# Kernel optimization log

Hardware: AMD Instinct MI355X
Metric: run time of the kernel (lower is better)

The kernel has to match this reference:

```python
import jax, jax.numpy as jnp
import numpy as np

B, T = 32768, 32
OBJ_V, PRED_V = 179, 46
E_OBJ, E_PRED, H = 5, 5, 32
IN_DIM = E_OBJ + E_PRED + 2 + 4  # 16, matches LSTMCell input size


def setup_inputs() -> dict:
    key = jax.random.key(0)
    ks = jax.random.split(key, 12)
    s = 0.1
    return {
        "input_objects": jax.random.randint(ks[0], (B, T), 0, OBJ_V),
        "input_boxes": jax.random.uniform(ks[1], (B, T, 4), dtype=jnp.float32),
        "predicates": jax.random.randint(ks[2], (B, T), 0, PRED_V),
        "subject_indicators": jax.random.randint(ks[3], (B, T), 0, 2),
        "target_object": jax.random.randint(ks[4], (B,), 0, OBJ_V),
        "obj_emb": jax.random.normal(ks[5], (OBJ_V, E_OBJ), dtype=jnp.float32) * s,
        "pred_emb": jax.random.normal(ks[6], (PRED_V, E_PRED), dtype=jnp.float32) * s,
        "W_ih": jax.random.normal(ks[7], (4 * H, IN_DIM), dtype=jnp.float32) * s,
        "W_hh": jax.random.normal(ks[8], (4 * H, H), dtype=jnp.float32) * s,
        "b_ih": jnp.zeros((4 * H,), dtype=jnp.float32),
        "b_hh": jnp.zeros((4 * H,), dtype=jnp.float32),
        "fc2_W": jax.random.normal(ks[9], (4, H), dtype=jnp.float32) * s,
        "fc2_b": jnp.zeros((4,), dtype=jnp.float32),
    }


def _forward(input_objects, input_boxes, predicates, subject_indicators,
             obj_emb, pred_emb, W_ih, W_hh, b_ih, b_hh, fc2_W, fc2_b):
    # concatenate_features, vectorized over all timesteps at once: [B,T,16]
    feats = jnp.concatenate([
        obj_emb[input_objects],                                   # [B,T,5]
        pred_emb[predicates],                                     # [B,T,5]
        jax.nn.one_hot(subject_indicators, 2, dtype=jnp.float32), # [B,T,2]
        input_boxes,                                              # [B,T,4]
    ], axis=-1)
    xs = jnp.transpose(feats, (1, 0, 2))  # [T,B,16] for scan over time

    def step(carry, x):
        h, c = carry
        gates = x @ W_ih.T + b_ih + h @ W_hh.T + b_hh  # [B,4H]
        i, f, g, o = jnp.split(gates, 4, axis=-1)      # torch gate order i,f,g,o
        i = jax.nn.sigmoid(i)
        f = jax.nn.sigmoid(f)
        g = jnp.tanh(g)
        o = jax.nn.sigmoid(o)
        c = f * c + i * g
        h = o * jnp.tanh(c)
        return (h, c), None

    h0 = jnp.zeros((input_objects.shape[0], H), dtype=jnp.float32)
    (h, _), _ = jax.lax.scan(step, (h0, h0), xs)
    out = h @ fc2_W.T + fc2_b          # output_fc2 on last hidden state
    return jnp.clip(out, 0.0, 1.0)     # torch.clamp(min=0, max=1)


def reference(input_objects, input_boxes, predicates, subject_indicators, target_object,
              obj_emb, pred_emb, W_ih, W_hh, b_ih, b_hh, fc2_W, fc2_b):
    # target_object is accepted by the torch forward but unused in its body
    return _forward(input_objects, input_boxes, predicates, subject_indicators,
                    obj_emb, pred_emb, W_ih, W_hh, b_ih, b_hh, fc2_W, fc2_b)
```

## Files before the change

kernel.cpp:

```cpp
#include <hip/hip_runtime.h>

#define LDS_BYTES 16656

typedef _Float16 f16x8 __attribute__((ext_vector_type(8)));
typedef float    f32x4 __attribute__((ext_vector_type(4)));

#define LOG2E     1.44269504088896f
#define TWO_LOG2E 2.88539008177793f

__device__ __forceinline__ float sig_pre(float a) {
    return __builtin_amdgcn_rcpf(1.0f + __builtin_amdgcn_exp2f(a));
}
__device__ __forceinline__ float tanh_pre(float a) {
    return 1.0f - 2.0f * __builtin_amdgcn_rcpf(1.0f + __builtin_amdgcn_exp2f(a));
}
__device__ __forceinline__ int pack2(float a, float b) {
    union { _Float16 h[2]; int i; } u;
    u.h[0] = (_Float16)a; u.h[1] = (_Float16)b;
    return u.i;
}

__global__ __launch_bounds__(64, 2)
void lstm_fused(const int* __restrict__ objs,
                const float* __restrict__ boxes,
                const int* __restrict__ preds,
                const int* __restrict__ subj,
                const float* __restrict__ obj_emb,
                const float* __restrict__ pred_emb,
                const float* __restrict__ W_ih,
                const float* __restrict__ W_hh,
                const float* __restrict__ b_ih,
                const float* __restrict__ b_hh,
                const float* __restrict__ fc2_W,
                const float* __restrict__ fc2_b,
                float* __restrict__ out)
{
    extern __shared__ char smem[];
    const int tid  = threadIdx.x;
    const int quad = tid >> 4;
    const int cidx = tid & 15;
    const int XOFF = 0, ZOFF = 16640;

    if (tid < 4) ((int*)(smem + ZOFF))[tid] = 0;

    {
        int b  = tid >> 2;
        int t0 = (tid & 3) << 3;
        long gb = (long)blockIdx.x * 16 + b;
        const int* op = objs  + gb * 32 + t0;
        const int* pp = preds + gb * 32 + t0;
        const int* sp = subj  + gb * 32 + t0;
        #pragma unroll
        for (int c = 0; c < 8; c += 4) {
            int4 ov = *(const int4*)(op + c);
            int4 pv = *(const int4*)(pp + c);
            int4 sv = *(const int4*)(sp + c);
            int oarr[4] = {ov.x, ov.y, ov.z, ov.w};
            int parr[4] = {pv.x, pv.y, pv.z, pv.w};
            int sarr[4] = {sv.x, sv.y, sv.z, sv.w};
            #pragma unroll
            for (int tt = 0; tt < 4; ++tt) {
                int t = t0 + c + tt;
                const float* eo = obj_emb  + oarr[tt] * 5;
                const float* ep = pred_emb + parr[tt] * 5;
                float4 bx = *(const float4*)(boxes + (gb * 32 + t) * 4);
                f16x8 lo, hi;
                lo[0]=(_Float16)eo[0]; lo[1]=(_Float16)eo[1]; lo[2]=(_Float16)eo[2];
                lo[3]=(_Float16)eo[3]; lo[4]=(_Float16)eo[4];
                lo[5]=(_Float16)ep[0]; lo[6]=(_Float16)ep[1]; lo[7]=(_Float16)ep[2];
                hi[0]=(_Float16)ep[3]; hi[1]=(_Float16)ep[4];
                hi[2]=(_Float16)(sarr[tt]==0 ? 1.0f : 0.0f);
                hi[3]=(_Float16)(sarr[tt]==1 ? 1.0f : 0.0f);
                hi[4]=(_Float16)bx.x; hi[5]=(_Float16)bx.y;
                hi[6]=(_Float16)bx.z; hi[7]=(_Float16)bx.w;
                char* dst = smem + XOFF + b * 1040 + t * 32;
                *(f16x8*)dst        = lo;
                *(f16x8*)(dst + 16) = hi;
            }
        }
    }

    f16x8 Wf[8][2];
    f32x4 bias4[8];
    #pragma unroll
    for (int j = 0; j < 8; ++j) {
        float scale = (j == 4 || j == 5) ? TWO_LOG2E : -LOG2E;
        int n = j * 16 + cidx;
        #pragma unroll
        for (int ks = 0; ks < 2; ++ks) {
            f16x8 v;
            #pragma unroll
            for (int jj = 0; jj < 8; ++jj) {
                int k = ks * 32 + quad * 8 + jj;
                float val = (k < 16) ? W_ih[n * 16 + k]
                          : (k >= 32) ? W_hh[n * 32 + (k - 32)]
                          : 0.0f;
                v[jj] = (_Float16)(val * scale);
            }
            Wf[j][ks] = v;
        }
        #pragma unroll
        for (int r = 0; r < 4; ++r) {
            int nr = j * 16 + quad * 4 + r;
            bias4[j][r] = (b_ih[nr] + b_hh[nr]) * scale;
        }
    }

    const bool qlow = (quad < 2);
    int       xaddr = qlow ? (XOFF + cidx * 1040 + quad * 16) : ZOFF;
    const int xinc  = qlow ? 32 : 0;
    const int idx_lo = (((quad & 1) << 5) + cidx) << 2;
    const int idx_hi = idx_lo + 64;

    __syncthreads();

    f16x8 xfrag = *(const f16x8*)(smem + xaddr); xaddr += xinc;
    f32x4 accp[8];
    #pragma unroll
    for (int j = 0; j < 8; ++j)
        accp[j] = __builtin_amdgcn_mfma_f32_16x16x32_f16(Wf[j][0], xfrag, bias4[j], 0, 0, 0);

    int pkA = 0, pkB = 0, pkC = 0, pkD = 0;
    float cst[8] = {0,0,0,0,0,0,0,0};
    float hl[8];

    #pragma unroll 4
    for (int t = 0; t < 32; ++t) {
        int pa_lo = __builtin_amdgcn_ds_bpermute(idx_lo, pkA);
        int pb_lo = __builtin_amdgcn_ds_bpermute(idx_lo, pkB);
        int pa_hi = __builtin_amdgcn_ds_bpermute(idx_hi, pkA);
        int pb_hi = __builtin_amdgcn_ds_bpermute(idx_hi, pkB);
        int pc_lo = __builtin_amdgcn_ds_bpermute(idx_lo, pkC);
        int pd_lo = __builtin_amdgcn_ds_bpermute(idx_lo, pkD);
        int pc_hi = __builtin_amdgcn_ds_bpermute(idx_hi, pkC);
        int pd_hi = __builtin_amdgcn_ds_bpermute(idx_hi, pkD);
        union { int i[4]; f16x8 v; } hf;
        hf.i[0] = qlow ? pa_lo : pc_lo;
        hf.i[1] = qlow ? pb_lo : pd_lo;
        hf.i[2] = qlow ? pa_hi : pc_hi;
        hf.i[3] = qlow ? pb_hi : pd_hi;

        f32x4 acc[8];
        #pragma unroll
        for (int j = 0; j < 8; ++j)
            acc[j] = __builtin_amdgcn_mfma_f32_16x16x32_f16(Wf[j][1], hf.v, accp[j], 0, 0, 0);

        f16x8 xn = *(const f16x8*)(smem + xaddr); xaddr += xinc;

        #pragma unroll
        for (int r = 0; r < 4; ++r) {
            float si0 = sig_pre(acc[0][r]);
            float si1 = sig_pre(acc[1][r]);
            float sf0 = sig_pre(acc[2][r]);
            float sf1 = sig_pre(acc[3][r]);
            float tg0 = tanh_pre(acc[4][r]);
            float tg1 = tanh_pre(acc[5][r]);
            float so0 = sig_pre(acc[6][r]);
            float so1 = sig_pre(acc[7][r]);
            float c0 = fmaf(sf0, cst[2*r],   si0 * tg0);
            float c1 = fmaf(sf1, cst[2*r+1], si1 * tg1);
            cst[2*r] = c0; cst[2*r+1] = c1;
            hl[2*r]   = so0 * tanh_pre(c0 * TWO_LOG2E);
            hl[2*r+1] = so1 * tanh_pre(c1 * TWO_LOG2E);
        }
        pkA = pack2(hl[0], hl[2]);
        pkB = pack2(hl[4], hl[6]);
        pkC = pack2(hl[1], hl[3]);
        pkD = pack2(hl[5], hl[7]);

        #pragma unroll
        for (int j = 0; j < 8; ++j)
            accp[j] = __builtin_amdgcn_mfma_f32_16x16x32_f16(Wf[j][0], xn, bias4[j], 0, 0, 0);
    }

    __syncthreads();
    #pragma unroll
    for (int r = 0; r < 4; ++r) {
        *(float*)(smem + cidx * 144 + (quad * 4 + r) * 4)        = hl[2*r];
        *(float*)(smem + cidx * 144 + (16 + quad * 4 + r) * 4)   = hl[2*r+1];
    }
    __syncthreads();

    {
        int b = tid >> 2, jj = tid & 3;
        const float* fw   = fc2_W + jj * 32;
        const float* hrow = (const float*)(smem + b * 144);
        float s = fc2_b[jj];
        #pragma unroll
        for (int k = 0; k < 8; ++k) {
            float4 hv = *(const float4*)(hrow + k * 4);
            s += fw[k*4+0] * hv.x + fw[k*4+1] * hv.y
               + fw[k*4+2] * hv.z + fw[k*4+3] * hv.w;
        }
        s = fminf(fmaxf(s, 0.0f), 1.0f);
        out[(long)blockIdx.x * 64 + tid] = s;
    }
}

extern "C" void kernel_launch(void* const* d_in, const int* in_sizes, int n_in,
                              void* d_out, int out_size, void* d_ws, size_t ws_size,
                              hipStream_t stream)
{
    lstm_fused<<<2048, 64, LDS_BYTES, stream>>>(
        (const int*)d_in[0], (const float*)d_in[1], (const int*)d_in[2],
        (const int*)d_in[3],
        (const float*)d_in[5], (const float*)d_in[6],
        (const float*)d_in[7], (const float*)d_in[8],
        (const float*)d_in[9], (const float*)d_in[10],
        (const float*)d_in[11], (const float*)d_in[12],
        (float*)d_out);
}
```

Before: 146.0 us.

## Permute gate weight rows so MFMA output feeds next step without lane shuffles

Each gate's weight rows and biases are reordered so that the hidden units a lane computes are exactly the ones it must supply as the B-fragment of the next recurrent MFMA. This removes the eight ds_bpermute cross-lane exchanges and their selects from the serial per-timestep dependency chain; h is packed directly into the fragment registers. The loop unroll factor also drops from 4 to 2 and a slightly larger zero region is reserved in LDS. The final hidden-state write-back is remapped to the new unit ordering.

After: 145.6 us. About the same (-0.2%).

```diff
diff --git a/kernel.cpp b/kernel.cpp
--- a/kernel.cpp
+++ b/kernel.cpp
@@ -1,6 +1,6 @@
 #include <hip/hip_runtime.h>
 
-#define LDS_BYTES 16656
+#define LDS_BYTES 16672
 
 typedef _Float16 f16x8 __attribute__((ext_vector_type(8)));
 typedef float    f32x4 __attribute__((ext_vector_type(4)));
@@ -41,7 +41,7 @@
     const int cidx = tid & 15;
     const int XOFF = 0, ZOFF = 16640;
 
-    if (tid < 4) ((int*)(smem + ZOFF))[tid] = 0;
+    if (tid < 8) ((int*)(smem + ZOFF))[tid] = 0;
 
     {
         int b  = tid >> 2;
@@ -84,8 +84,10 @@
     f32x4 bias4[8];
     #pragma unroll
     for (int j = 0; j < 8; ++j) {
-        float scale = (j == 4 || j == 5) ? TWO_LOG2E : -LOG2E;
-        int n = j * 16 + cidx;
+        int g = j >> 1, half = j & 1;
+        float scale = (g == 2) ? TWO_LOG2E : -LOG2E;
+        int um = 8 * (cidx >> 2) + (cidx & 3) + 4 * half;
+        int n  = g * 32 + um;
         #pragma unroll
         for (int ks = 0; ks < 2; ++ks) {
             f16x8 v;
@@ -101,16 +103,14 @@
         }
         #pragma unroll
         for (int r = 0; r < 4; ++r) {
-            int nr = j * 16 + quad * 4 + r;
-            bias4[j][r] = (b_ih[nr] + b_hh[nr]) * scale;
+            int ur = 8 * quad + r + 4 * half;
+            bias4[j][r] = (b_ih[g * 32 + ur] + b_hh[g * 32 + ur]) * scale;
         }
     }
 
     const bool qlow = (quad < 2);
     int       xaddr = qlow ? (XOFF + cidx * 1040 + quad * 16) : ZOFF;
     const int xinc  = qlow ? 32 : 0;
-    const int idx_lo = (((quad & 1) << 5) + cidx) << 2;
-    const int idx_hi = idx_lo + 64;
 
     __syncthreads();
 
@@ -120,25 +120,14 @@
     for (int j = 0; j < 8; ++j)
         accp[j] = __builtin_amdgcn_mfma_f32_16x16x32_f16(Wf[j][0], xfrag, bias4[j], 0, 0, 0);
 
-    int pkA = 0, pkB = 0, pkC = 0, pkD = 0;
+    int pk0 = 0, pk1 = 0, pk2 = 0, pk3 = 0;
     float cst[8] = {0,0,0,0,0,0,0,0};
-    float hl[8];
-
-    #pragma unroll 4
+    float h_lo[4], h_hi[4];
+
+    #pragma unroll 2
     for (int t = 0; t < 32; ++t) {
-        int pa_lo = __builtin_amdgcn_ds_bpermute(idx_lo, pkA);
-        int pb_lo = __builtin_amdgcn_ds_bpermute(idx_lo, pkB);
-        int pa_hi = __builtin_amdgcn_ds_bpermute(idx_hi, pkA);
-        int pb_hi = __builtin_amdgcn_ds_bpermute(idx_hi, pkB);
-        int pc_lo = __builtin_amdgcn_ds_bpermute(idx_lo, pkC);
-        int pd_lo = __builtin_amdgcn_ds_bpermute(idx_lo, pkD);
-        int pc_hi = __builtin_amdgcn_ds_bpermute(idx_hi, pkC);
-        int pd_hi = __builtin_amdgcn_ds_bpermute(idx_hi, pkD);
         union { int i[4]; f16x8 v; } hf;
-        hf.i[0] = qlow ? pa_lo : pc_lo;
-        hf.i[1] = qlow ? pb_lo : pd_lo;
-        hf.i[2] = qlow ? pa_hi : pc_hi;
-        hf.i[3] = qlow ? pb_hi : pd_hi;
+        hf.i[0] = pk0; hf.i[1] = pk1; hf.i[2] = pk2; hf.i[3] = pk3;
 
         f32x4 acc[8];
         #pragma unroll
@@ -149,24 +138,24 @@
 
         #pragma unroll
         for (int r = 0; r < 4; ++r) {
-            float si0 = sig_pre(acc[0][r]);
-            float si1 = sig_pre(acc[1][r]);
-            float sf0 = sig_pre(acc[2][r]);
-            float sf1 = sig_pre(acc[3][r]);
-            float tg0 = tanh_pre(acc[4][r]);
-            float tg1 = tanh_pre(acc[5][r]);
-            float so0 = sig_pre(acc[6][r]);
-            float so1 = sig_pre(acc[7][r]);
-            float c0 = fmaf(sf0, cst[2*r],   si0 * tg0);
-            float c1 = fmaf(sf1, cst[2*r+1], si1 * tg1);
-            cst[2*r] = c0; cst[2*r+1] = c1;
-            hl[2*r]   = so0 * tanh_pre(c0 * TWO_LOG2E);
-            hl[2*r+1] = so1 * tanh_pre(c1 * TWO_LOG2E);
-        }
-        pkA = pack2(hl[0], hl[2]);
-        pkB = pack2(hl[4], hl[6]);
-        pkC = pack2(hl[1], hl[3]);
-        pkD = pack2(hl[5], hl[7]);
+            float i0 = sig_pre(acc[0][r]);
+            float i1 = sig_pre(acc[1][r]);
+            float f0 = sig_pre(acc[2][r]);
+            float f1 = sig_pre(acc[3][r]);
+            float g0 = tanh_pre(acc[4][r]);
+            float g1 = tanh_pre(acc[5][r]);
+            float o0 = sig_pre(acc[6][r]);
+            float o1 = sig_pre(acc[7][r]);
+            float c0 = fmaf(f0, cst[r],     i0 * g0);
+            float c1 = fmaf(f1, cst[4 + r], i1 * g1);
+            cst[r] = c0; cst[4 + r] = c1;
+            h_lo[r] = o0 * tanh_pre(c0 * TWO_LOG2E);
+            h_hi[r] = o1 * tanh_pre(c1 * TWO_LOG2E);
+        }
+        pk0 = pack2(h_lo[0], h_lo[1]);
+        pk1 = pack2(h_lo[2], h_lo[3]);
+        pk2 = pack2(h_hi[0], h_hi[1]);
+        pk3 = pack2(h_hi[2], h_hi[3]);
 
         #pragma unroll
         for (int j = 0; j < 8; ++j)
@@ -176,8 +165,8 @@
     __syncthreads();
     #pragma unroll
     for (int r = 0; r < 4; ++r) {
-        *(float*)(smem + cidx * 144 + (quad * 4 + r) * 4)        = hl[2*r];
-        *(float*)(smem + cidx * 144 + (16 + quad * 4 + r) * 4)   = hl[2*r+1];
+        *(float*)(smem + cidx * 144 + (8 * quad + r) * 4)     = h_lo[r];
+        *(float*)(smem + cidx * 144 + (8 * quad + 4 + r) * 4) = h_hi[r];
     }
     __syncthreads();
 
```
